# Kernel optimization log

Hardware: AMD Instinct MI355X
Metric: run time of the kernel (lower is better)

The kernel has to match this reference:

```python
import jax, jax.numpy as jnp
import numpy as np

LN_EPS = 1e-5


def layer_norm(x, gamma, beta):
    mu = jnp.mean(x, axis=-1, keepdims=True)
    var = jnp.mean(jnp.square(x - mu), axis=-1, keepdims=True)
    return (x - mu) * jax.lax.rsqrt(var + LN_EPS) * gamma + beta


def setup_inputs() -> dict:
    key = jax.random.key(0)
    ks = jax.random.split(key, 4)
    b, t, d, h, r = 4, 2048, 1024, 4096, 32
    x = jax.random.normal(ks[0], (b, t, d), dtype=jnp.float32)
    L = jax.random.normal(ks[1], (d, r), dtype=jnp.float32) * (1.0 / np.sqrt(d))
    W1 = jax.random.normal(ks[2], (d, h), dtype=jnp.float32) * (1.0 / np.sqrt(d))
    W2 = jax.random.normal(ks[3], (h, d), dtype=jnp.float32) * (1.0 / np.sqrt(h))
    return {
        "x": x, "L": L,
        "W1": W1, "b1": jnp.zeros((h,), jnp.float32),
        "W2": W2, "b2": jnp.zeros((d,), jnp.float32),
        "gamma1": jnp.ones((d,), jnp.float32), "beta1": jnp.zeros((d,), jnp.float32),
        "gamma2": jnp.ones((d,), jnp.float32), "beta2": jnp.zeros((d,), jnp.float32),
    }


def reference(x, L, W1, b1, W2, b2, gamma1, beta1, gamma2, beta2):
    d = x.shape[-1]
    # --- GeodesicAttention on norm1(x) ---
    hn = layer_norm(x, gamma1, beta1)  # (b,t,d)
    g = jnp.eye(d, dtype=x.dtype) + L @ L.T  # PSD metric G = I + L L^T, (d,d)
    # dist_sq[b,i,j] = (x_i - x_j)^T G (x_i - x_j)
    #               = q_i + q_j - 2 x_i^T G x_j   (quadratic expansion; avoids (b,t,t,d) diff tensor)
    xg = jnp.einsum('btd,de->bte', hn, g)          # G x, (b,t,d)
    q = jnp.einsum('btd,btd->bt', xg, hn)          # diag quadratic form, (b,t)
    cross = jnp.einsum('bid,bjd->bij', xg, hn)     # x_i^T G x_j, (b,t,t)
    dist_sq = q[:, :, None] + q[:, None, :] - 2.0 * cross
    attn = jax.nn.softmax(-dist_sq, axis=-1)       # (b,t,t)
    x = x + jnp.einsum('bij,bjd->bid', attn, hn)
    # --- MLP on norm2(x) ---
    hm = layer_norm(x, gamma2, beta2)
    hid = jax.nn.gelu(hm @ W1 + b1, approximate=False)
    x = x + hid @ W2 + b2
    return x
```

## Files before the change

### kernel.cpp

```cpp
#include <hip/hip_runtime.h>
#include <cstdint>

typedef float f32x4 __attribute__((ext_vector_type(4)));
typedef __bf16 bf16x8 __attribute__((ext_vector_type(8)));

#define AS1 __attribute__((address_space(1)))
#define AS3 __attribute__((address_space(3)))

__device__ __forceinline__ void gld_lds16(const void* g, void* l) {
    __builtin_amdgcn_global_load_lds((const AS1 void*)g, (AS3 void*)l, 16, 0, 0);
}

__device__ __forceinline__ unsigned short f2bf(float f) {
    unsigned u = __builtin_bit_cast(unsigned, f);
    u = u + 0x7fffu + ((u >> 16) & 1u);
    return (unsigned short)(u >> 16);
}
__device__ __forceinline__ float bf2f(unsigned short h) {
    unsigned u = ((unsigned)h) << 16;
    return __builtin_bit_cast(float, u);
}

__device__ __forceinline__ void bar() {
    asm volatile("" ::: "memory");
    __builtin_amdgcn_s_barrier();
    asm volatile("" ::: "memory");
}

#define WAITVM(n) asm volatile("s_waitcnt vmcnt(" #n ")" ::: "memory")
#define LGKM0     asm volatile("s_waitcnt lgkmcnt(0)" ::: "memory")
#define SCHED0    __builtin_amdgcn_sched_barrier(0)

template<int MODE>
__global__ __launch_bounds__(256, 3) void gemm128(
    const unsigned short* __restrict__ A, long lda, long sAb,
    const unsigned short* __restrict__ B, long ldb, long sBb,
    void* C, long ldc, long sCb,
    const float* add, long ldadd, long sAddb,
    const float* __restrict__ bias, int K)
{
    constexpr int ABUF = 128 * 64;
    constexpr int BUF  = 2 * ABUF;
    __shared__ char sm[3 * BUF];
    const int tid = threadIdx.x, lane = tid & 63, wid = tid >> 6;
    const int wr = wid >> 1, wc = wid & 1;

    const long zb = blockIdx.z;
    const int nwg  = gridDim.x * gridDim.y;
    const int orig = blockIdx.y * gridDim.x + blockIdx.x;
    const int q8 = nwg >> 3, r8 = nwg & 7;
    const int xcd = orig & 7;
    const int wg  = (xcd < r8 ? xcd * (q8 + 1) : r8 * (q8 + 1) + (xcd - r8) * q8) + (orig >> 3);
    const int bx = wg % gridDim.x, by = wg / gridDim.x;

    const char* Ab = (const char*)(A + zb * sAb + (long)by * 128 * lda);
    const char* Bb = (const char*)(B + zb * sBb + (long)bx * 128 * ldb);
    const long ldaB = lda * 2, ldbB = ldb * 2;

    const long gsw = (long)(((tid & 3) ^ ((tid >> 3) & 3)) << 4);
    auto stage = [&](int kt, int b) {
#pragma unroll
        for (int i = 0; i < 2; ++i) {
            const int r = i * 64 + (tid >> 2);
            gld_lds16(Ab + (long)r * ldaB + (long)kt * 64 + gsw,
                      sm + b * BUF + i * 4096 + wid * 1024);
            gld_lds16(Bb + (long)r * ldbB + (long)kt * 64 + gsw,
                      sm + b * BUF + ABUF + i * 4096 + wid * 1024);
        }
    };

    f32x4 acc[4][4] = {};
    const int NT = K / 32;
    const int cc = ((lane >> 4) ^ ((lane >> 1) & 3)) << 4;

    stage(0, 0); stage(1, 1);
    WAITVM(4);
    bar();

#pragma unroll 1
    for (int t = 0; t < NT; ++t) {
        const char* bufp = sm + (t % 3) * BUF;
        bf16x8 af[4], bfr[4];
#pragma unroll
        for (int m = 0; m < 4; ++m) {
            const int R = wr * 64 + m * 16 + (lane & 15);
            af[m] = *(const bf16x8*)(bufp + R * 64 + cc);
        }
#pragma unroll
        for (int n = 0; n < 4; ++n) {
            const int R = wc * 64 + n * 16 + (lane & 15);
            bfr[n] = *(const bf16x8*)(bufp + ABUF + R * 64 + cc);
        }
        if (t + 2 < NT) stage(t + 2, (t + 2) % 3);
        LGKM0; SCHED0;
        __builtin_amdgcn_s_setprio(1);
#pragma unroll
        for (int m = 0; m < 4; ++m)
#pragma unroll
            for (int n = 0; n < 4; ++n)
                acc[m][n] = __builtin_amdgcn_mfma_f32_16x16x32_bf16(
                    af[m], bfr[n], acc[m][n], 0, 0, 0);
        __builtin_amdgcn_s_setprio(0);
        if (t + 1 < NT) {
            if (t + 2 < NT) WAITVM(4); else WAITVM(0);
            bar();
        }
    }

    const long row0 = (long)by * 128 + wr * 64 + (lane >> 4) * 4;
    const long col0 = (long)bx * 128 + wc * 64 + (lane & 15);
#pragma unroll
    for (int m = 0; m < 4; ++m)
#pragma unroll
        for (int n = 0; n < 4; ++n)
#pragma unroll
            for (int j = 0; j < 4; ++j) {
                const long r = row0 + m * 16 + j;
                const long c = col0 + n * 16;
                const float v = acc[m][n][j];
                if (MODE == 0) {
                    ((float*)C)[zb * sCb + r * ldc + c] = v;
                } else if (MODE == 1) {
                    ((float*)C)[zb * sCb + r * ldc + c] = v + add[zb * sAddb + r * ldadd + c];
                } else if (MODE == 2) {
                    float tt = v + bias[c];
                    float gl = 0.5f * tt * (1.0f + erff(tt * 0.70710678118654752f));
                    ((unsigned short*)C)[zb * sCb + r * ldc + c] = f2bf(gl);
                } else {
                    ((float*)C)[zb * sCb + r * ldc + c] = v + bias[c] + add[zb * sAddb + r * ldadd + c];
                }
            }
}

__global__ __launch_bounds__(256) void ln_kernel(
    const float* __restrict__ x, const float* __restrict__ gamma, const float* __restrict__ beta,
    unsigned short* __restrict__ out, int ldout, float* qout, int pad)
{
    const int tid = threadIdx.x;
    const long row = blockIdx.x;
    float4 v = ((const float4*)(x + row * 1024))[tid];
    float s = v.x + v.y + v.z + v.w;
    float s2 = v.x * v.x + v.y * v.y + v.z * v.z + v.w * v.w;
#pragma unroll
    for (int off = 32; off; off >>= 1) {
        s  += __shfl_down(s, off);
        s2 += __shfl_down(s2, off);
    }
    __shared__ float red[12];
    const int lane = tid & 63, wid = tid >> 6;
    if (lane == 0) { red[wid] = s; red[4 + wid] = s2; }
    __syncthreads();
    s  = red[0] + red[1] + red[2] + red[3];
    s2 = red[4] + red[5] + red[6] + red[7];
    const float mu = s * (1.0f / 1024.0f);
    const float var = s2 * (1.0f / 1024.0f) - mu * mu;
    const float rs = rsqrtf(var + 1e-5f);
    const float4 g = ((const float4*)gamma)[tid];
    const float4 b = ((const float4*)beta)[tid];
    unsigned short o0 = f2bf((v.x - mu) * rs * g.x + b.x);
    unsigned short o1 = f2bf((v.y - mu) * rs * g.y + b.y);
    unsigned short o2 = f2bf((v.z - mu) * rs * g.z + b.z);
    unsigned short o3 = f2bf((v.w - mu) * rs * g.w + b.w);
    ushort4 ov; ov.x = o0; ov.y = o1; ov.z = o2; ov.w = o3;
    ((ushort4*)(out + row * (long)ldout))[tid] = ov;
    if (pad && tid < 32) out[row * (long)ldout + 1056 + tid] = 0;
    if (qout) {
        float y0 = bf2f(o0), y1 = bf2f(o1), y2 = bf2f(o2), y3 = bf2f(o3);
        float sq = y0 * y0 + y1 * y1 + y2 * y2 + y3 * y3;
#pragma unroll
        for (int off = 32; off; off >>= 1) sq += __shfl_down(sq, off);
        if (lane == 0) red[8 + wid] = sq;
        __syncthreads();
        if (tid == 0) qout[row] = red[8] + red[9] + red[10] + red[11];
    }
}

__global__ __launch_bounds__(256) void u_kernel(
    unsigned short* __restrict__ z, const float* __restrict__ L, float* __restrict__ q)
{
    const int tid = threadIdx.x;
    const long row = blockIdx.x;
    __shared__ float hn[1024];
    __shared__ float part[8][32];
    ushort4 uv = ((const ushort4*)(z + row * 1088))[tid];
    hn[tid * 4 + 0] = bf2f(uv.x);
    hn[tid * 4 + 1] = bf2f(uv.y);
    hn[tid * 4 + 2] = bf2f(uv.z);
    hn[tid * 4 + 3] = bf2f(uv.w);
    __syncthreads();
    const int j = tid & 31, grp = tid >> 5;
    float acc = 0.f;
    const float* Lp = L + j;
#pragma unroll 4
    for (int d = grp * 128; d < grp * 128 + 128; ++d)
        acc += hn[d] * Lp[(long)d * 32];
    part[grp][j] = acc;
    __syncthreads();
    if (tid < 32) {
        float u = 0.f;
#pragma unroll
        for (int g2 = 0; g2 < 8; ++g2) u += part[g2][tid];
        unsigned short ub = f2bf(u);
        z[row * 1088 + 1024 + tid] = ub;
        float uf = bf2f(ub);
        part[0][tid] = uf * uf;
    }
    __syncthreads();
    if (tid == 0) {
        float sq = 0.f;
#pragma unroll
        for (int t2 = 0; t2 < 32; ++t2) sq += part[0][t2];
        q[row] += sq;
    }
}

__global__ __launch_bounds__(256) void softmax_kernel(
    float* S, const float* qb)
{
    const int tid = threadIdx.x;
    const long i = blockIdx.x, bl = blockIdx.y;
    float* Sr = S + (bl * 2048 + i) * 2048;
    const float* qr = qb + bl * 2048;
    float l[8];
    float mx = -1e30f;
#pragma unroll
    for (int c2 = 0; c2 < 8; ++c2) {
        const int jj = tid + c2 * 256;
        l[c2] = 2.0f * Sr[jj] - qr[jj];
        mx = fmaxf(mx, l[c2]);
    }
#pragma unroll
    for (int off = 32; off; off >>= 1) mx = fmaxf(mx, __shfl_xor(mx, off));
    __shared__ float red[8];
    const int lane = tid & 63, wid = tid >> 6;
    if (lane == 0) red[wid] = mx;
    __syncthreads();
    mx = fmaxf(fmaxf(red[0], red[1]), fmaxf(red[2], red[3]));
    float sum = 0.f;
#pragma unroll
    for (int c2 = 0; c2 < 8; ++c2) { l[c2] = __expf(l[c2] - mx); sum += l[c2]; }
#pragma unroll
    for (int off = 32; off; off >>= 1) sum += __shfl_xor(sum, off);
    if (lane == 0) red[4 + wid] = sum;
    __syncthreads();
    sum = red[4] + red[5] + red[6] + red[7];
    const float inv = 1.0f / sum;
    unsigned short* Pr = (unsigned short*)S + (bl * 2048 + i) * 4096;
#pragma unroll
    for (int c2 = 0; c2 < 8; ++c2)
        Pr[tid + c2 * 256] = f2bf(l[c2] * inv);
}

__global__ __launch_bounds__(256) void transpose_v_kernel(
    const unsigned short* __restrict__ z, unsigned short* __restrict__ Vt, long sVtb)
{
    __shared__ unsigned short t[32][33];
    const int tid = threadIdx.x;
    const int tx = tid & 31, ty = tid >> 5;
    const long b = blockIdx.z;
    const long k0 = (long)blockIdx.x * 32, n0 = (long)blockIdx.y * 32;
#pragma unroll
    for (int r = 0; r < 32; r += 8)
        t[r + ty][tx] = z[(b * 2048 + k0 + r + ty) * 1088 + n0 + tx];
    __syncthreads();
#pragma unroll
    for (int r = 0; r < 32; r += 8)
        Vt[b * sVtb + (n0 + r + ty) * 2048 + k0 + tx] = t[tx][r + ty];
}

__global__ __launch_bounds__(256) void cast_transpose_kernel(
    const float* __restrict__ W, unsigned short* __restrict__ Wt, int rows, int cols)
{
    __shared__ float t[32][33];
    const int tid = threadIdx.x;
    const int tx = tid & 31, ty = tid >> 5;
    const long r0 = (long)blockIdx.y * 32, c0 = (long)blockIdx.x * 32;
#pragma unroll
    for (int r = 0; r < 32; r += 8)
        t[r + ty][tx] = W[(r0 + r + ty) * (long)cols + c0 + tx];
    __syncthreads();
#pragma unroll
    for (int r = 0; r < 32; r += 8)
        Wt[(c0 + r + ty) * (long)rows + r0 + tx] = f2bf(t[tx][r + ty]);
}

extern "C" void kernel_launch(void* const* d_in, const int* in_sizes, int n_in,
                              void* d_out, int out_size, void* d_ws, size_t ws_size,
                              hipStream_t stream)
{
    const float* x   = (const float*)d_in[0];
    const float* L   = (const float*)d_in[1];
    const float* W1  = (const float*)d_in[2];
    const float* b1  = (const float*)d_in[3];
    const float* W2  = (const float*)d_in[4];
    const float* b2  = (const float*)d_in[5];
    const float* g1  = (const float*)d_in[6];
    const float* be1 = (const float*)d_in[7];
    const float* g2  = (const float*)d_in[8];
    const float* be2 = (const float*)d_in[9];
    float* out = (float*)d_out;
    unsigned short* z = (unsigned short*)d_out;

    char* wsp = (char*)d_ws;
    float* q = (float*)wsp;
    char* pool = wsp + 32768;
    unsigned short* Vt   = (unsigned short*)pool;
    float*          Smat = (float*)(pool + 16777216);
    unsigned short* W1t = (unsigned short*)pool;
    unsigned short* W2t = (unsigned short*)(pool + 8388608);
    unsigned short* hm  = (unsigned short*)(pool + 16777216);
    unsigned short* hid = (unsigned short*)(pool + 33554432);
    const bool fullMLP = ws_size >= (size_t)32768 + 100663296 + 65536;

    ln_kernel<<<8192, 256, 0, stream>>>(x, g1, be1, z, 1088, q, 1);
    u_kernel<<<8192, 256, 0, stream>>>(z, L, q);

    transpose_v_kernel<<<dim3(64, 32, 4), 256, 0, stream>>>(z, Vt, (long)1024 * 2048);
    gemm128<0><<<dim3(16, 16, 4), 256, 0, stream>>>(
        z, 1088, (long)2048 * 1088,
        z, 1088, (long)2048 * 1088,
        Smat, 2048, (long)2048 * 2048,
        nullptr, 0, 0, nullptr, 1088);
    softmax_kernel<<<dim3(2048, 4), 256, 0, stream>>>(Smat, q);
    gemm128<1><<<dim3(8, 16, 4), 256, 0, stream>>>(
        (const unsigned short*)Smat, 4096, (long)2048 * 4096,
        Vt, 2048, (long)1024 * 2048,
        out, 1024, (long)2048 * 1024,
        x, 1024, (long)2048 * 1024,
        nullptr, 2048);

    cast_transpose_kernel<<<dim3(128, 32), 256, 0, stream>>>(W1, W1t, 1024, 4096);
    cast_transpose_kernel<<<dim3(32, 128), 256, 0, stream>>>(W2, W2t, 4096, 1024);
    ln_kernel<<<8192, 256, 0, stream>>>(out, g2, be2, hm, 1024, nullptr, 0);
    if (fullMLP) {
        gemm128<2><<<dim3(32, 64, 1), 256, 0, stream>>>(
            hm, 1024, 0, W1t, 1024, 0,
            hid, 4096, 0, nullptr, 0, 0, b1, 1024);
        gemm128<3><<<dim3(8, 64, 1), 256, 0, stream>>>(
            hid, 4096, 0, W2t, 4096, 0,
            out, 1024, 0, out, 1024, 0, b2, 4096);
    } else {
        for (int c = 0; c < 2; ++c) {
            const unsigned short* hmc = hm + (size_t)c * 4096 * 1024;
            float* oc = out + (size_t)c * 4096 * 1024;
            gemm128<2><<<dim3(32, 32, 1), 256, 0, stream>>>(
                hmc, 1024, 0, W1t, 1024, 0,
                hid, 4096, 0, nullptr, 0, 0, b1, 1024);
            gemm128<3><<<dim3(8, 32, 1), 256, 0, stream>>>(
                hid, 4096, 0, W2t, 4096, 0,
                oc, 1024, 0, oc, 1024, 0, b2, 4096);
        }
    }
}
```

Baseline: 392.6 us.

## Compute only lower-triangular tiles of symmetric cross-product GEMM and mirror results

The cross GEMM (z·zᵀ with an augmented K=1088) yields a symmetric score matrix, so it now launches only the 136 lower-triangular 128x128 tiles per batch instead of 256. Each off-diagonal tile also writes its transposed accumulator to the mirrored position. This roughly halves the MFMA work and operand loads for this GEMM, at the cost of extra strided transposed stores and a small loop to map block index to tile coordinates.

```diff
diff --git a/kernel.cpp b/kernel.cpp
--- a/kernel.cpp
+++ b/kernel.cpp
@@ -31,7 +31,7 @@
 #define LGKM0     asm volatile("s_waitcnt lgkmcnt(0)" ::: "memory")
 #define SCHED0    __builtin_amdgcn_sched_barrier(0)
 
-template<int MODE>
+template<int MODE, int TRI>
 __global__ __launch_bounds__(256, 3) void gemm128(
     const unsigned short* __restrict__ A, long lda, long sAb,
     const unsigned short* __restrict__ B, long ldb, long sBb,
@@ -51,7 +51,17 @@
     const int q8 = nwg >> 3, r8 = nwg & 7;
     const int xcd = orig & 7;
     const int wg  = (xcd < r8 ? xcd * (q8 + 1) : r8 * (q8 + 1) + (xcd - r8) * q8) + (orig >> 3);
-    const int bx = wg % gridDim.x, by = wg / gridDim.x;
+    int bx, by;
+    if constexpr (TRI == 1) {
+        int k = 0;
+        while (2 * (k + 1) * (k + 1) + (k + 1) <= wg) ++k;
+        const int i = wg - (2 * k * k + k);
+        const int R = 2 * k;
+        if (i < 2 * (R + 1)) { by = R + (i & 1); bx = i >> 1; }
+        else                 { by = R + 1;      bx = R + 1;  }
+    } else {
+        bx = wg % gridDim.x; by = wg / gridDim.x;
+    }
 
     const char* Ab = (const char*)(A + zb * sAb + (long)by * 128 * lda);
     const char* Bb = (const char*)(B + zb * sBb + (long)bx * 128 * ldb);
@@ -130,6 +140,17 @@
                     ((float*)C)[zb * sCb + r * ldc + c] = v + bias[c] + add[zb * sAddb + r * ldadd + c];
                 }
             }
+    if constexpr (TRI == 1) {
+        if (by != bx) {
+#pragma unroll
+            for (int m = 0; m < 4; ++m)
+#pragma unroll
+                for (int n = 0; n < 4; ++n) {
+                    float* dst = (float*)C + zb * sCb + (col0 + n * 16) * ldc + (row0 + m * 16);
+                    *(float4*)dst = (float4){acc[m][n][0], acc[m][n][1], acc[m][n][2], acc[m][n][3]};
+                }
+        }
+    }
 }
 
 __global__ __launch_bounds__(256) void ln_kernel(
@@ -316,13 +337,13 @@
     u_kernel<<<8192, 256, 0, stream>>>(z, L, q);
 
     transpose_v_kernel<<<dim3(64, 32, 4), 256, 0, stream>>>(z, Vt, (long)1024 * 2048);
-    gemm128<0><<<dim3(16, 16, 4), 256, 0, stream>>>(
+    gemm128<0, 1><<<dim3(136, 1, 4), 256, 0, stream>>>(
         z, 1088, (long)2048 * 1088,
         z, 1088, (long)2048 * 1088,
         Smat, 2048, (long)2048 * 2048,
         nullptr, 0, 0, nullptr, 1088);
     softmax_kernel<<<dim3(2048, 4), 256, 0, stream>>>(Smat, q);
-    gemm128<1><<<dim3(8, 16, 4), 256, 0, stream>>>(
+    gemm128<1, 0><<<dim3(8, 16, 4), 256, 0, stream>>>(
         (const unsigned short*)Smat, 4096, (long)2048 * 4096,
         Vt, 2048, (long)1024 * 2048,
         out, 1024, (long)2048 * 1024,
@@ -333,20 +354,20 @@
     cast_transpose_kernel<<<dim3(32, 128), 256, 0, stream>>>(W2, W2t, 4096, 1024);
     ln_kernel<<<8192, 256, 0, stream>>>(out, g2, be2, hm, 1024, nullptr, 0);
     if (fullMLP) {
-        gemm128<2><<<dim3(32, 64, 1), 256, 0, stream>>>(
+        gemm128<2, 0><<<dim3(32, 64, 1), 256, 0, stream>>>(
             hm, 1024, 0, W1t, 1024, 0,
             hid, 4096, 0, nullptr, 0, 0, b1, 1024);
-        gemm128<3><<<dim3(8, 64, 1), 256, 0, stream>>>(
+        gemm128<3, 0><<<dim3(8, 64, 1), 256, 0, stream>>>(
             hid, 4096, 0, W2t, 4096, 0,
             out, 1024, 0, out, 1024, 0, b2, 4096);
     } else {
         for (int c = 0; c < 2; ++c) {
             const unsigned short* hmc = hm + (size_t)c * 4096 * 1024;
             float* oc = out + (size_t)c * 4096 * 1024;
-            gemm128<2><<<dim3(32, 32, 1), 256, 0, stream>>>(
+            gemm128<2, 0><<<dim3(32, 32, 1), 256, 0, stream>>>(
                 hmc, 1024, 0, W1t, 1024, 0,
                 hid, 4096, 0, nullptr, 0, 0, b1, 1024);
-            gemm128<3><<<dim3(8, 32, 1), 256, 0, stream>>>(
+            gemm128<3, 0><<<dim3(8, 32, 1), 256, 0, stream>>>(
                 hid, 4096, 0, W2t, 4096, 0,
                 oc, 1024, 0, oc, 1024, 0, b2, 4096);
         }
```

Measured after the change: 383.2 us. 2.4% less time.
